# Kernel optimization log

Measured on AMD Instinct MI355X. Metric: run time of the kernel, lower is better.

The kernel has to match this reference:

```python
import jax, jax.numpy as jnp
import numpy as np

B, T, L, R, E, F = 8, 16, 128, 1024, 5, 512
# range(min_dist_exp, max_dist_exp+1) with 0 removed, per Diffusion.__init__
DIST_EXPONENTS = jnp.array([-3.0, -2.0, -1.0, 1.0, 2.0], dtype=jnp.float32)


def setup_inputs() -> dict:
    key = jax.random.key(0)
    ks = jax.random.split(key, 8)
    return {
        "lig_feat": jax.random.normal(ks[0], (B, L, E, F), jnp.float32) * 0.1,
        "rec_feat": jax.random.normal(ks[1], (B, R, E, F), jnp.float32) * 0.1,
        # coords on ~angstrom scale so negative-power distances stay bounded
        "lig_coord": jax.random.normal(ks[2], (B, L, 3), jnp.float32) * 5.0,
        "rec_coord": jax.random.normal(ks[3], (B, R, 3), jnp.float32) * 5.0,
        "pre_rot": jax.random.normal(ks[4], (B, T, 3, 3), jnp.float32),
        "trans": jax.random.normal(ks[5], (B, T, 3), jnp.float32),
        "lig_counts": jax.random.randint(ks[6], (B,), L // 2, L + 1, jnp.int32),
        "rec_counts": jax.random.randint(ks[7], (B,), R // 2, R + 1, jnp.int32),
    }


def reference(lig_feat, rec_feat, lig_coord, rec_coord, pre_rot, trans,
              lig_counts, rec_counts):
    # get_energy over a ragged batch (padded + masked), vectorized over
    # graphs (b) and timesteps (t). rot = QR(pre_rot) as in energy_grad.
    exps = DIST_EXPONENTS.astype(lig_feat.dtype)          # [E]
    rot = jnp.linalg.qr(pre_rot)[0]                       # [B,T,3,3]
    # einsum('nij,bj->nbi', rot, lig_coord) + trans, batched over graphs
    new_lig = jnp.einsum('btij,blj->btli', rot, lig_coord) + trans[:, :, None, :]  # [B,T,L,3]

    lig_mask = jnp.arange(lig_coord.shape[1]) < lig_counts[:, None]   # [B,L]
    rec_mask = jnp.arange(rec_coord.shape[1]) < rec_counts[:, None]   # [B,R]
    pair_mask = lig_mask[:, :, None] & rec_mask[:, None, :]           # [B,L,R]

    # atn_coefs = einsum('lef,ref->lre'); zero out padded pairs
    atn = jnp.einsum('blef,bref->blre', lig_feat, rec_feat) * pair_mask[..., None]  # [B,L,R,E]

    diff = new_lig[:, :, :, None, :] - rec_coord[:, None, None, :, :]  # [B,T,L,R,3]
    dists = jnp.sqrt(jnp.sum(diff * diff, axis=-1))                    # [B,T,L,R]
    # padded pairs -> 1.0 so negative exponents don't produce inf*0
    dists = jnp.where(pair_mask[:, None, :, :], dists, 1.0)
    dist_exp = dists[..., None] ** exps                                # [B,T,L,R,E]

    U = jnp.einsum('blre,btlre->bt', atn, dist_exp)                    # [B,T]
    return U
```

## Files before the change

kernel.cpp:

```cpp
#include <hip/hip_runtime.h>
#include <hip/hip_bf16.h>

#define B_ 8
#define T_ 16
#define L_ 128
#define R_ 1024
#define E_ 5
#define F_ 512

typedef short short8 __attribute__((ext_vector_type(8)));
typedef float floatx4 __attribute__((ext_vector_type(4)));
typedef unsigned short ushort4v __attribute__((ext_vector_type(4)));

__device__ __forceinline__ unsigned short f2bf(float f) {
  unsigned u = __float_as_uint(f);
  return (unsigned short)((u + 0x8000u) >> 16);
}

__device__ __forceinline__ short8 pack8(floatx4 lo, floatx4 hi) {
  short8 v;
  v[0] = (short)f2bf(lo[0]); v[1] = (short)f2bf(lo[1]);
  v[2] = (short)f2bf(lo[2]); v[3] = (short)f2bf(lo[3]);
  v[4] = (short)f2bf(hi[0]); v[5] = (short)f2bf(hi[1]);
  v[6] = (short)f2bf(hi[2]); v[7] = (short)f2bf(hi[3]);
  return v;
}

__device__ __forceinline__ void stage16(const float* g, float* lds) {
  __builtin_amdgcn_global_load_lds(
      (const __attribute__((address_space(1))) void*)g,
      (__attribute__((address_space(3))) void*)lds, 16, 0, 0);
}

#define WAITCNT_VM6 0xF76
#define WAITCNT_VM0 0xF70

__global__ void prep_kernel(const float* __restrict__ lig_coord,
                            const float* __restrict__ pre_rot,
                            const float* __restrict__ trans,
                            float* __restrict__ new_lig) {
  int bt = blockIdx.x;
  __shared__ float Qs[3][3];
  if (threadIdx.x == 0) {
    float a[3][3], q[3][3];
    #pragma unroll
    for (int i = 0; i < 3; ++i)
      #pragma unroll
      for (int j = 0; j < 3; ++j) {
        a[i][j] = pre_rot[(bt * 3 + i) * 3 + j];
        q[i][j] = (i == j) ? 1.f : 0.f;
      }
    for (int k = 0; k < 3; ++k) {
      float alpha = a[k][k];
      float xn2 = 0.f;
      for (int i = k + 1; i < 3; ++i) xn2 += a[i][k] * a[i][k];
      float nrm = sqrtf(alpha * alpha + xn2);
      if (xn2 > 0.f && nrm > 0.f) {
        float beta = (alpha >= 0.f) ? -nrm : nrm;
        float tau = (beta - alpha) / beta;
        float inv = 1.f / (alpha - beta);
        float v[3] = {0.f, 0.f, 0.f};
        v[k] = 1.f;
        for (int i = k + 1; i < 3; ++i) v[i] = a[i][k] * inv;
        for (int j = k; j < 3; ++j) {
          float w = 0.f;
          for (int i = k; i < 3; ++i) w += v[i] * a[i][j];
          w *= tau;
          for (int i = k; i < 3; ++i) a[i][j] -= w * v[i];
        }
        for (int i = 0; i < 3; ++i) {
          float w = 0.f;
          for (int j = k; j < 3; ++j) w += q[i][j] * v[j];
          w *= tau;
          for (int j = k; j < 3; ++j) q[i][j] -= w * v[j];
        }
      }
    }
    for (int i = 0; i < 3; ++i)
      for (int j = 0; j < 3; ++j) Qs[i][j] = q[i][j];
  }
  __syncthreads();
  int b = bt >> 4;
  int l = threadIdx.x;
  float cx = lig_coord[(b * L_ + l) * 3 + 0];
  float cy = lig_coord[(b * L_ + l) * 3 + 1];
  float cz = lig_coord[(b * L_ + l) * 3 + 2];
  float nx = Qs[0][0] * cx + Qs[0][1] * cy + Qs[0][2] * cz + trans[bt * 3 + 0];
  float ny = Qs[1][0] * cx + Qs[1][1] * cy + Qs[1][2] * cz + trans[bt * 3 + 1];
  float nz = Qs[2][0] * cx + Qs[2][1] * cy + Qs[2][2] * cz + trans[bt * 3 + 2];
  float* o = new_lig + ((size_t)bt * L_ + l) * 3;
  o[0] = nx; o[1] = ny; o[2] = nz;
}

__launch_bounds__(256)
__global__ void gemm_kernel(const float* __restrict__ lig_feat,
                            const float* __restrict__ rec_feat,
                            const int* __restrict__ rec_counts,
                            unsigned short* __restrict__ atn) {
  const int rt = blockIdx.x;
  const int e  = blockIdx.y;
  const int b  = blockIdx.z;
  const int r0 = rt * 64;
  if (r0 >= rec_counts[b]) return;

  __shared__ float As[2][128 * 32];
  __shared__ float Bs[2][64 * 32];

  const int tid  = threadIdx.x;
  const int wave = tid >> 6;
  const int lane = tid & 63;
  const int lrow = lane & 15;
  const int quad = lane >> 4;
  const int wm   = wave * 32;

  const int lr8 = lane >> 3;
  const int sw  = (lane & 7) ^ lr8;
  const float* ga[4];
  #pragma unroll
  for (int i = 0; i < 4; ++i) {
    int row = wave * 32 + i * 8 + lr8;
    ga[i] = lig_feat + ((size_t)(b * L_ + row) * E_ + e) * F_ + sw * 4;
  }
  const float* gb[2];
  #pragma unroll
  for (int i = 0; i < 2; ++i) {
    int row = wave * 16 + i * 8 + lr8;
    gb[i] = rec_feat + ((size_t)(b * R_ + r0 + row) * E_ + e) * F_ + sw * 4;
  }

  floatx4 acc[2][4];
  #pragma unroll
  for (int i = 0; i < 2; ++i)
    #pragma unroll
    for (int j = 0; j < 4; ++j)
      acc[i][j] = (floatx4){0.f, 0.f, 0.f, 0.f};

  const int c0 = (2 * quad) ^ (lane & 7);

  #pragma unroll
  for (int i = 0; i < 4; ++i) stage16(ga[i], &As[0][(wave * 32 + i * 8) * 32]);
  #pragma unroll
  for (int i = 0; i < 2; ++i) stage16(gb[i], &Bs[0][(wave * 16 + i * 8) * 32]);

  #pragma unroll 1
  for (int kc = 0; kc < 16; ++kc) {
    const int cur = kc & 1;
    if (kc > 0)
      __builtin_amdgcn_s_barrier();
    if (kc < 15) {
      const int col = (kc + 1) * 32;
      #pragma unroll
      for (int i = 0; i < 4; ++i)
        stage16(ga[i] + col, &As[cur ^ 1][(wave * 32 + i * 8) * 32]);
      #pragma unroll
      for (int i = 0; i < 2; ++i)
        stage16(gb[i] + col, &Bs[cur ^ 1][(wave * 16 + i * 8) * 32]);
      __builtin_amdgcn_s_waitcnt(WAITCNT_VM6);
    } else {
      __builtin_amdgcn_s_waitcnt(WAITCNT_VM0);
    }
    __builtin_amdgcn_s_barrier();
    __builtin_amdgcn_sched_barrier(0);

    short8 af[2], bfv[4];
    #pragma unroll
    for (int i = 0; i < 2; ++i) {
      const float* base = &As[cur][(wm + i * 16 + lrow) * 32];
      af[i] = pack8(*(const floatx4*)(base + c0 * 4),
                    *(const floatx4*)(base + (c0 ^ 1) * 4));
    }
    #pragma unroll
    for (int j = 0; j < 4; ++j) {
      const float* base = &Bs[cur][(j * 16 + lrow) * 32];
      bfv[j] = pack8(*(const floatx4*)(base + c0 * 4),
                     *(const floatx4*)(base + (c0 ^ 1) * 4));
    }
    #pragma unroll
    for (int i = 0; i < 2; ++i)
      #pragma unroll
      for (int j = 0; j < 4; ++j)
        acc[i][j] = __builtin_amdgcn_mfma_f32_16x16x32_bf16(af[i], bfv[j], acc[i][j], 0, 0, 0);
  }

  const size_t base = (size_t)(b * E_ + e) * L_ * R_;
  #pragma unroll
  for (int i = 0; i < 2; ++i)
    #pragma unroll
    for (int j = 0; j < 4; ++j)
      #pragma unroll
      for (int reg = 0; reg < 4; ++reg) {
        int m = wm + i * 16 + quad * 4 + reg;
        int n = j * 16 + lrow;
        atn[base + (size_t)m * R_ + r0 + n] = f2bf(acc[i][j][reg]);
      }
}

__launch_bounds__(256)
__global__ void reduce_kernel(const unsigned short* __restrict__ atn,
                              const float* __restrict__ new_lig,
                              const float* __restrict__ rec_coord,
                              const int* __restrict__ lig_counts,
                              const int* __restrict__ rec_counts,
                              float* __restrict__ partial) {
  const int b = blockIdx.x >> 7;
  const int l = blockIdx.x & 127;
  const int tid = threadIdx.x;
  if (l >= lig_counts[b]) {
    if (tid < T_) partial[(size_t)(b * T_ + tid) * L_ + l] = 0.f;
    return;
  }
  const int recN = rec_counts[b];
  const int wave = tid >> 6;

  __shared__ float nl[T_][3];
  __shared__ float sm[4][T_];
  if (tid < T_ * 3)
    nl[tid / 3][tid % 3] =
        new_lig[((size_t)(b * T_ + tid / 3) * L_ + l) * 3 + (tid % 3)];
  __syncthreads();

  float u[T_];
  #pragma unroll
  for (int t = 0; t < T_; ++t) u[t] = 0.f;

  if (wave * 256 < recN) {
    const int r = tid * 4;
    const size_t plane = (size_t)L_ * R_;
    const unsigned short* atnB = atn + (size_t)b * E_ * plane + (size_t)l * R_ + r;
    const float* rcB = rec_coord + ((size_t)b * R_ + r) * 3;

    ushort4v a4[5];
    #pragma unroll
    for (int e = 0; e < 5; ++e) a4[e] = *(const ushort4v*)(atnB + e * plane);
    floatx4 q0 = *(const floatx4*)(rcB + 0);
    floatx4 q1 = *(const floatx4*)(rcB + 4);
    floatx4 q2 = *(const floatx4*)(rcB + 8);
    float px[4] = {q0[0], q0[3], q1[2], q2[1]};
    float py[4] = {q0[1], q1[0], q1[3], q2[2]};
    float pz[4] = {q0[2], q1[1], q2[0], q2[3]};
    float am[5][4];
    #pragma unroll
    for (int e = 0; e < 5; ++e)
      #pragma unroll
      for (int s = 0; s < 4; ++s)
        am[e][s] = (r + s < recN)
                       ? __uint_as_float((unsigned)a4[e][s] << 16)
                       : 0.f;

    #pragma unroll
    for (int t = 0; t < T_; ++t) {
      float acc = 0.f;
      #pragma unroll
      for (int s = 0; s < 4; ++s) {
        float dx = nl[t][0] - px[s];
        float dy = nl[t][1] - py[s];
        float dz = nl[t][2] - pz[s];
        float d2 = fmaf(dx, dx, fmaf(dy, dy, dz * dz));
        d2 = fmaxf(d2, 1e-20f);
        float rs  = rsqrtf(d2);
        float rs2 = rs * rs;
        float rs3 = rs2 * rs;
        float d1  = d2 * rs;
        float c = am[0][s] * rs3;
        c = fmaf(am[1][s], rs2, c);
        c = fmaf(am[2][s], rs, c);
        c = fmaf(am[3][s], d1, c);
        c = fmaf(am[4][s], d2, c);
        acc += c;
      }
      u[t] += acc;
    }
  }

  #pragma unroll
  for (int t = 0; t < T_; ++t) {
    float v = u[t];
    #pragma unroll
    for (int m = 32; m > 0; m >>= 1) v += __shfl_xor(v, m, 64);
    if ((tid & 63) == 0) sm[wave][t] = v;
  }
  __syncthreads();
  if (tid < T_)
    partial[(size_t)(b * T_ + tid) * L_ + l] =
        sm[0][tid] + sm[1][tid] + sm[2][tid] + sm[3][tid];
}

__global__ void final_kernel(const float* __restrict__ partial,
                             float* __restrict__ out) {
  const int bt = blockIdx.x;
  const int l = threadIdx.x;
  float v = partial[(size_t)bt * L_ + l];
  #pragma unroll
  for (int m = 32; m > 0; m >>= 1) v += __shfl_xor(v, m, 64);
  __shared__ float s[2];
  if ((l & 63) == 0) s[l >> 6] = v;
  __syncthreads();
  if (l == 0) out[bt] = s[0] + s[1];
}

extern "C" void kernel_launch(void* const* d_in, const int* in_sizes, int n_in,
                              void* d_out, int out_size, void* d_ws, size_t ws_size,
                              hipStream_t stream) {
  const float* lig_feat   = (const float*)d_in[0];
  const float* rec_feat   = (const float*)d_in[1];
  const float* lig_coord  = (const float*)d_in[2];
  const float* rec_coord  = (const float*)d_in[3];
  const float* pre_rot    = (const float*)d_in[4];
  const float* trans      = (const float*)d_in[5];
  const int*   lig_counts = (const int*)d_in[6];
  const int*   rec_counts = (const int*)d_in[7];
  float* out = (float*)d_out;

  float* new_lig = (float*)d_ws;
  unsigned short* atn = (unsigned short*)(new_lig + (size_t)B_ * T_ * L_ * 3);
  float* partial = (float*)(atn + (size_t)B_ * E_ * L_ * R_);

  prep_kernel<<<dim3(B_ * T_), dim3(L_), 0, stream>>>(lig_coord, pre_rot, trans, new_lig);
  gemm_kernel<<<dim3(R_ / 64, E_, B_), dim3(256), 0, stream>>>(lig_feat, rec_feat,
                                                               rec_counts, atn);
  reduce_kernel<<<dim3(B_ * L_), dim3(256), 0, stream>>>(atn, new_lig, rec_coord,
                                                         lig_counts, rec_counts, partial);
  final_kernel<<<dim3(B_ * T_), dim3(128), 0, stream>>>(partial, out);
}
```

Before: 167.5 us.

## Fuse attention GEMM with distance-energy reduction and atomically accumulate output

Merges the bf16 MFMA GEMM and the distance-power reduction into one kernel. Each block computes all five exponent channels for a 128x32 ligand-receptor tile, keeps the results in registers, and evaluates the energy terms directly, so the bf16 atn intermediate is never written to or read from global memory. Per-block sums are added into the output with atomicAdd after prep zeroes it, which removes the partial and final kernels. The trade-off is fewer, larger blocks (256 instead of 640 GEMM blocks) that each run a longer sequential K loop, plus heavier register pressure from holding the accumulators of all five channels.

New measurement: 212.4 us. 1.27x slower.

```diff
diff --git a/kernel.cpp b/kernel.cpp
--- a/kernel.cpp
+++ b/kernel.cpp
@@ -1,5 +1,4 @@
 #include <hip/hip_runtime.h>
-#include <hip/hip_bf16.h>
 
 #define B_ 8
 #define T_ 16
@@ -10,7 +9,6 @@
 
 typedef short short8 __attribute__((ext_vector_type(8)));
 typedef float floatx4 __attribute__((ext_vector_type(4)));
-typedef unsigned short ushort4v __attribute__((ext_vector_type(4)));
 
 __device__ __forceinline__ unsigned short f2bf(float f) {
   unsigned u = __float_as_uint(f);
@@ -32,16 +30,19 @@
       (__attribute__((address_space(3))) void*)lds, 16, 0, 0);
 }
 
-#define WAITCNT_VM6 0xF76
+#define WAITCNT_VM3 0xF73
+#define WAITCNT_VM2 0xF72
 #define WAITCNT_VM0 0xF70
 
 __global__ void prep_kernel(const float* __restrict__ lig_coord,
                             const float* __restrict__ pre_rot,
                             const float* __restrict__ trans,
-                            float* __restrict__ new_lig) {
+                            float* __restrict__ new_lig,
+                            float* __restrict__ out) {
   int bt = blockIdx.x;
   __shared__ float Qs[3][3];
   if (threadIdx.x == 0) {
+    out[bt] = 0.f;
     float a[3][3], q[3][3];
     #pragma unroll
     for (int i = 0; i < 3; ++i)
@@ -92,184 +93,165 @@
   o[0] = nx; o[1] = ny; o[2] = nz;
 }
 
-__launch_bounds__(256)
-__global__ void gemm_kernel(const float* __restrict__ lig_feat,
-                            const float* __restrict__ rec_feat,
-                            const int* __restrict__ rec_counts,
-                            unsigned short* __restrict__ atn) {
+__launch_bounds__(512)
+__global__ void fused_kernel(const float* __restrict__ lig_feat,
+                             const float* __restrict__ rec_feat,
+                             const float* __restrict__ rec_coord,
+                             const int* __restrict__ lig_counts,
+                             const int* __restrict__ rec_counts,
+                             const float* __restrict__ new_lig,
+                             float* __restrict__ out) {
   const int rt = blockIdx.x;
-  const int e  = blockIdx.y;
-  const int b  = blockIdx.z;
-  const int r0 = rt * 64;
-  if (r0 >= rec_counts[b]) return;
-
-  __shared__ float As[2][128 * 32];
-  __shared__ float Bs[2][64 * 32];
+  const int b  = blockIdx.y;
+  const int r0 = rt * 32;
+  const int recN = rec_counts[b];
+  if (r0 >= recN) return;
+
+  __shared__ __align__(16) float smem[2 * 128 * 32 + 2 * 32 * 32];
+  __shared__ float smr[8][T_];
+  float* const As0 = smem;
+  float* const Bs0 = smem + 2 * 128 * 32;
 
   const int tid  = threadIdx.x;
   const int wave = tid >> 6;
   const int lane = tid & 63;
   const int lrow = lane & 15;
   const int quad = lane >> 4;
-  const int wm   = wave * 32;
+  const int wm   = wave * 16;
 
   const int lr8 = lane >> 3;
   const int sw  = (lane & 7) ^ lr8;
-  const float* ga[4];
-  #pragma unroll
-  for (int i = 0; i < 4; ++i) {
-    int row = wave * 32 + i * 8 + lr8;
-    ga[i] = lig_feat + ((size_t)(b * L_ + row) * E_ + e) * F_ + sw * 4;
-  }
-  const float* gb[2];
+  const bool bwave = (wave < 4);
+
+  const float* ga[2];
   #pragma unroll
   for (int i = 0; i < 2; ++i) {
     int row = wave * 16 + i * 8 + lr8;
-    gb[i] = rec_feat + ((size_t)(b * R_ + r0 + row) * E_ + e) * F_ + sw * 4;
-  }
-
-  floatx4 acc[2][4];
-  #pragma unroll
-  for (int i = 0; i < 2; ++i)
-    #pragma unroll
-    for (int j = 0; j < 4; ++j)
-      acc[i][j] = (floatx4){0.f, 0.f, 0.f, 0.f};
+    ga[i] = lig_feat + ((size_t)(b * L_ + row) * E_) * F_ + sw * 4;
+  }
+  const float* gb = rec_feat +
+      ((size_t)(b * R_ + r0 + wave * 8 + lr8) * E_) * F_ + sw * 4;
+
+  const int dstA0 = (wave * 16 + 0) * 32;
+  const int dstA1 = (wave * 16 + 8) * 32;
+  const int dstB  = (wave * 8) * 32;
+
+  floatx4 acc[E_][2];
+  #pragma unroll
+  for (int e = 0; e < E_; ++e)
+    #pragma unroll
+    for (int j = 0; j < 2; ++j)
+      acc[e][j] = (floatx4){0.f, 0.f, 0.f, 0.f};
+
+  stage16(ga[0], As0 + dstA0);
+  stage16(ga[1], As0 + dstA1);
+  if (bwave) stage16(gb, Bs0 + dstB);
 
   const int c0 = (2 * quad) ^ (lane & 7);
 
   #pragma unroll
-  for (int i = 0; i < 4; ++i) stage16(ga[i], &As[0][(wave * 32 + i * 8) * 32]);
-  #pragma unroll
-  for (int i = 0; i < 2; ++i) stage16(gb[i], &Bs[0][(wave * 16 + i * 8) * 32]);
-
-  #pragma unroll 1
-  for (int kc = 0; kc < 16; ++kc) {
-    const int cur = kc & 1;
-    if (kc > 0)
+  for (int e = 0; e < E_; ++e) {
+    #pragma unroll 1
+    for (int kc = 0; kc < 16; ++kc) {
+      const int g = e * 16 + kc;
+      const int cur = g & 1;
+      if (g > 0)
+        __builtin_amdgcn_s_barrier();
+      if (g < 79) {
+        const int col = (g + 1) * 32;
+        stage16(ga[0] + col, As0 + (cur ^ 1) * (128 * 32) + dstA0);
+        stage16(ga[1] + col, As0 + (cur ^ 1) * (128 * 32) + dstA1);
+        if (bwave) {
+          stage16(gb + col, Bs0 + (cur ^ 1) * (32 * 32) + dstB);
+          __builtin_amdgcn_s_waitcnt(WAITCNT_VM3);
+        } else {
+          __builtin_amdgcn_s_waitcnt(WAITCNT_VM2);
+        }
+      } else {
+        __builtin_amdgcn_s_waitcnt(WAITCNT_VM0);
+      }
       __builtin_amdgcn_s_barrier();
-    if (kc < 15) {
-      const int col = (kc + 1) * 32;
-      #pragma unroll
-      for (int i = 0; i < 4; ++i)
-        stage16(ga[i] + col, &As[cur ^ 1][(wave * 32 + i * 8) * 32]);
-      #pragma unroll
-      for (int i = 0; i < 2; ++i)
-        stage16(gb[i] + col, &Bs[cur ^ 1][(wave * 16 + i * 8) * 32]);
-      __builtin_amdgcn_s_waitcnt(WAITCNT_VM6);
-    } else {
-      __builtin_amdgcn_s_waitcnt(WAITCNT_VM0);
-    }
-    __builtin_amdgcn_s_barrier();
-    __builtin_amdgcn_sched_barrier(0);
-
-    short8 af[2], bfv[4];
-    #pragma unroll
-    for (int i = 0; i < 2; ++i) {
-      const float* base = &As[cur][(wm + i * 16 + lrow) * 32];
-      af[i] = pack8(*(const floatx4*)(base + c0 * 4),
-                    *(const floatx4*)(base + (c0 ^ 1) * 4));
-    }
-    #pragma unroll
-    for (int j = 0; j < 4; ++j) {
-      const float* base = &Bs[cur][(j * 16 + lrow) * 32];
-      bfv[j] = pack8(*(const floatx4*)(base + c0 * 4),
-                     *(const floatx4*)(base + (c0 ^ 1) * 4));
-    }
-    #pragma unroll
-    for (int i = 0; i < 2; ++i)
-      #pragma unroll
-      for (int j = 0; j < 4; ++j)
-        acc[i][j] = __builtin_amdgcn_mfma_f32_16x16x32_bf16(af[i], bfv[j], acc[i][j], 0, 0, 0);
-  }
-
-  const size_t base = (size_t)(b * E_ + e) * L_ * R_;
-  #pragma unroll
-  for (int i = 0; i < 2; ++i)
-    #pragma unroll
-    for (int j = 0; j < 4; ++j)
+      __builtin_amdgcn_sched_barrier(0);
+
+      const float* abase = As0 + cur * (128 * 32) + (wm + lrow) * 32;
+      short8 af = pack8(*(const floatx4*)(abase + c0 * 4),
+                        *(const floatx4*)(abase + (c0 ^ 1) * 4));
+      const float* bbase0 = Bs0 + cur * (32 * 32) + (lrow) * 32;
+      const float* bbase1 = Bs0 + cur * (32 * 32) + (16 + lrow) * 32;
+      short8 bf0 = pack8(*(const floatx4*)(bbase0 + c0 * 4),
+                         *(const floatx4*)(bbase0 + (c0 ^ 1) * 4));
+      short8 bf1 = pack8(*(const floatx4*)(bbase1 + c0 * 4),
+                         *(const floatx4*)(bbase1 + (c0 ^ 1) * 4));
+      acc[e][0] = __builtin_amdgcn_mfma_f32_16x16x32_bf16(af, bf0, acc[e][0], 0, 0, 0);
+      acc[e][1] = __builtin_amdgcn_mfma_f32_16x16x32_bf16(af, bf1, acc[e][1], 0, 0, 0);
+    }
+  }
+
+  __syncthreads();
+
+
+  float* const nlp = smem;
+  {
+    const floatx4* src = (const floatx4*)(new_lig + (size_t)b * T_ * L_ * 3);
+    floatx4* dst = (floatx4*)nlp;
+    #pragma unroll
+    for (int i = 0; i < 3; ++i) dst[tid + i * 512] = src[tid + i * 512];
+  }
+  __syncthreads();
+
+  const int ligN = lig_counts[b];
+  #pragma unroll
+  for (int j = 0; j < 2; ++j) {
+    const bool nv = (r0 + j * 16 + lrow) < recN;
+    #pragma unroll
+    for (int reg = 0; reg < 4; ++reg) {
+      const bool mv = (wm + quad * 4 + reg) < ligN;
+      if (!(nv && mv)) {
+        #pragma unroll
+        for (int e = 0; e < E_; ++e) acc[e][j][reg] = 0.f;
+      }
+    }
+  }
+
+  float rcx[2], rcy[2], rcz[2];
+  #pragma unroll
+  for (int j = 0; j < 2; ++j) {
+    const float* rp = rec_coord + (size_t)(b * R_ + r0 + j * 16 + lrow) * 3;
+    rcx[j] = rp[0]; rcy[j] = rp[1]; rcz[j] = rp[2];
+  }
+
+  float u[T_];
+  #pragma unroll
+  for (int t = 0; t < T_; ++t) u[t] = 0.f;
+
+  #pragma unroll
+  for (int t = 0; t < T_; ++t) {
+    float nx[4], ny[4], nz[4];
+    #pragma unroll
+    for (int reg = 0; reg < 4; ++reg) {
+      const float* np = nlp + ((t * L_) + wm + quad * 4 + reg) * 3;
+      nx[reg] = np[0]; ny[reg] = np[1]; nz[reg] = np[2];
+    }
+    #pragma unroll
+    for (int j = 0; j < 2; ++j)
       #pragma unroll
       for (int reg = 0; reg < 4; ++reg) {
-        int m = wm + i * 16 + quad * 4 + reg;
-        int n = j * 16 + lrow;
-        atn[base + (size_t)m * R_ + r0 + n] = f2bf(acc[i][j][reg]);
-      }
-}
-
-__launch_bounds__(256)
-__global__ void reduce_kernel(const unsigned short* __restrict__ atn,
-                              const float* __restrict__ new_lig,
-                              const float* __restrict__ rec_coord,
-                              const int* __restrict__ lig_counts,
-                              const int* __restrict__ rec_counts,
-                              float* __restrict__ partial) {
-  const int b = blockIdx.x >> 7;
-  const int l = blockIdx.x & 127;
-  const int tid = threadIdx.x;
-  if (l >= lig_counts[b]) {
-    if (tid < T_) partial[(size_t)(b * T_ + tid) * L_ + l] = 0.f;
-    return;
-  }
-  const int recN = rec_counts[b];
-  const int wave = tid >> 6;
-
-  __shared__ float nl[T_][3];
-  __shared__ float sm[4][T_];
-  if (tid < T_ * 3)
-    nl[tid / 3][tid % 3] =
-        new_lig[((size_t)(b * T_ + tid / 3) * L_ + l) * 3 + (tid % 3)];
-  __syncthreads();
-
-  float u[T_];
-  #pragma unroll
-  for (int t = 0; t < T_; ++t) u[t] = 0.f;
-
-  if (wave * 256 < recN) {
-    const int r = tid * 4;
-    const size_t plane = (size_t)L_ * R_;
-    const unsigned short* atnB = atn + (size_t)b * E_ * plane + (size_t)l * R_ + r;
-    const float* rcB = rec_coord + ((size_t)b * R_ + r) * 3;
-
-    ushort4v a4[5];
-    #pragma unroll
-    for (int e = 0; e < 5; ++e) a4[e] = *(const ushort4v*)(atnB + e * plane);
-    floatx4 q0 = *(const floatx4*)(rcB + 0);
-    floatx4 q1 = *(const floatx4*)(rcB + 4);
-    floatx4 q2 = *(const floatx4*)(rcB + 8);
-    float px[4] = {q0[0], q0[3], q1[2], q2[1]};
-    float py[4] = {q0[1], q1[0], q1[3], q2[2]};
-    float pz[4] = {q0[2], q1[1], q2[0], q2[3]};
-    float am[5][4];
-    #pragma unroll
-    for (int e = 0; e < 5; ++e)
-      #pragma unroll
-      for (int s = 0; s < 4; ++s)
-        am[e][s] = (r + s < recN)
-                       ? __uint_as_float((unsigned)a4[e][s] << 16)
-                       : 0.f;
-
-    #pragma unroll
-    for (int t = 0; t < T_; ++t) {
-      float acc = 0.f;
-      #pragma unroll
-      for (int s = 0; s < 4; ++s) {
-        float dx = nl[t][0] - px[s];
-        float dy = nl[t][1] - py[s];
-        float dz = nl[t][2] - pz[s];
+        float dx = nx[reg] - rcx[j];
+        float dy = ny[reg] - rcy[j];
+        float dz = nz[reg] - rcz[j];
         float d2 = fmaf(dx, dx, fmaf(dy, dy, dz * dz));
         d2 = fmaxf(d2, 1e-20f);
         float rs  = rsqrtf(d2);
         float rs2 = rs * rs;
         float rs3 = rs2 * rs;
         float d1  = d2 * rs;
-        float c = am[0][s] * rs3;
-        c = fmaf(am[1][s], rs2, c);
-        c = fmaf(am[2][s], rs, c);
-        c = fmaf(am[3][s], d1, c);
-        c = fmaf(am[4][s], d2, c);
-        acc += c;
-      }
-      u[t] += acc;
-    }
+        float c = acc[0][j][reg] * rs3;
+        c = fmaf(acc[1][j][reg], rs2, c);
+        c = fmaf(acc[2][j][reg], rs,  c);
+        c = fmaf(acc[3][j][reg], d1,  c);
+        c = fmaf(acc[4][j][reg], d2,  c);
+        u[t] += c;
+      }
   }
 
   #pragma unroll
@@ -277,25 +259,15 @@
     float v = u[t];
     #pragma unroll
     for (int m = 32; m > 0; m >>= 1) v += __shfl_xor(v, m, 64);
-    if ((tid & 63) == 0) sm[wave][t] = v;
-  }
-  __syncthreads();
-  if (tid < T_)
-    partial[(size_t)(b * T_ + tid) * L_ + l] =
-        sm[0][tid] + sm[1][tid] + sm[2][tid] + sm[3][tid];
-}
-
-__global__ void final_kernel(const float* __restrict__ partial,
-                             float* __restrict__ out) {
-  const int bt = blockIdx.x;
-  const int l = threadIdx.x;
-  float v = partial[(size_t)bt * L_ + l];
-  #pragma unroll
-  for (int m = 32; m > 0; m >>= 1) v += __shfl_xor(v, m, 64);
-  __shared__ float s[2];
-  if ((l & 63) == 0) s[l >> 6] = v;
-  __syncthreads();
-  if (l == 0) out[bt] = s[0] + s[1];
+    if (lane == 0) smr[wave][t] = v;
+  }
+  __syncthreads();
+  if (tid < T_) {
+    float s = 0.f;
+    #pragma unroll
+    for (int w = 0; w < 8; ++w) s += smr[w][tid];
+    atomicAdd(&out[b * T_ + tid], s);
+  }
 }
 
 extern "C" void kernel_launch(void* const* d_in, const int* in_sizes, int n_in,
@@ -312,13 +284,9 @@
   float* out = (float*)d_out;
 
   float* new_lig = (float*)d_ws;
-  unsigned short* atn = (unsigned short*)(new_lig + (size_t)B_ * T_ * L_ * 3);
-  float* partial = (float*)(atn + (size_t)B_ * E_ * L_ * R_);
-
-  prep_kernel<<<dim3(B_ * T_), dim3(L_), 0, stream>>>(lig_coord, pre_rot, trans, new_lig);
-  gemm_kernel<<<dim3(R_ / 64, E_, B_), dim3(256), 0, stream>>>(lig_feat, rec_feat,
-                                                               rec_counts, atn);
-  reduce_kernel<<<dim3(B_ * L_), dim3(256), 0, stream>>>(atn, new_lig, rec_coord,
-                                                         lig_counts, rec_counts, partial);
-  final_kernel<<<dim3(B_ * T_), dim3(128), 0, stream>>>(partial, out);
-}
+
+  prep_kernel<<<dim3(B_ * T_), dim3(L_), 0, stream>>>(lig_coord, pre_rot, trans,
+                                                      new_lig, out);
+  fused_kernel<<<dim3(R_ / 32, B_), dim3(512), 0, stream>>>(
+      lig_feat, rec_feat, rec_coord, lig_counts, rec_counts, new_lig, out);
+}
```

## Fuse distance-power reduction into GEMM epilogue with atomic output accumulation

Applied to the files above, without the earlier changes.

Removes the bf16 attention intermediate and the separate reduce and final kernels. Each GEMM block now computes distance powers for its own exponent directly on the MFMA accumulators and accumulates per-timestep sums into the output with atomics. The output is zeroed in the prep kernel. This avoids writing and re-reading the 10 MB atn buffer and cuts two launches, but it adds redundant distance computation per exponent block, LDS staging of new_lig, syncthreads per timestep group, and float atomics with nondeterministic summation order.

Result: slower. 180.5 us (+7.7%).

```diff
diff --git a/kernel.cpp b/kernel.cpp
--- a/kernel.cpp
+++ b/kernel.cpp
@@ -1,5 +1,4 @@
 #include <hip/hip_runtime.h>
-#include <hip/hip_bf16.h>
 
 #define B_ 8
 #define T_ 16
@@ -10,7 +9,6 @@
 
 typedef short short8 __attribute__((ext_vector_type(8)));
 typedef float floatx4 __attribute__((ext_vector_type(4)));
-typedef unsigned short ushort4v __attribute__((ext_vector_type(4)));
 
 __device__ __forceinline__ unsigned short f2bf(float f) {
   unsigned u = __float_as_uint(f);
@@ -38,10 +36,12 @@
 __global__ void prep_kernel(const float* __restrict__ lig_coord,
                             const float* __restrict__ pre_rot,
                             const float* __restrict__ trans,
-                            float* __restrict__ new_lig) {
+                            float* __restrict__ new_lig,
+                            float* __restrict__ out) {
   int bt = blockIdx.x;
   __shared__ float Qs[3][3];
   if (threadIdx.x == 0) {
+    out[bt] = 0.f;
     float a[3][3], q[3][3];
     #pragma unroll
     for (int i = 0; i < 3; ++i)
@@ -92,19 +92,75 @@
   o[0] = nx; o[1] = ny; o[2] = nz;
 }
 
+template <int EIDX>
+__device__ __forceinline__ void phaseB(const floatx4 (&acc)[2][4],
+                                       const float* nlp,
+                                       const float (&rcx)[4],
+                                       const float (&rcy)[4],
+                                       const float (&rcz)[4],
+                                       int wm, int quad, int lane, int wave,
+                                       float (*smr)[T_]) {
+  #pragma unroll 1
+  for (int tg = 0; tg < 4; ++tg) {
+    #pragma unroll
+    for (int it = 0; it < 4; ++it) {
+      const int t = tg * 4 + it;
+      float uacc = 0.f;
+      #pragma unroll
+      for (int i = 0; i < 2; ++i)
+        #pragma unroll
+        for (int reg = 0; reg < 4; ++reg) {
+          const int m = wm + i * 16 + quad * 4 + reg;
+          const float* np = nlp + (t * L_ + m) * 3;
+          const float nx = np[0], ny = np[1], nz = np[2];
+          #pragma unroll
+          for (int j = 0; j < 4; ++j) {
+            float dx = nx - rcx[j];
+            float dy = ny - rcy[j];
+            float dz = nz - rcz[j];
+            float d2 = fmaf(dx, dx, fmaf(dy, dy, dz * dz));
+            d2 = fmaxf(d2, 1e-20f);
+            float p;
+            if constexpr (EIDX == 0) {
+              float rs = rsqrtf(d2); p = rs * rs * rs;
+            } else if constexpr (EIDX == 1) {
+              float rs = rsqrtf(d2); p = rs * rs;
+            } else if constexpr (EIDX == 2) {
+              p = rsqrtf(d2);
+            } else if constexpr (EIDX == 3) {
+              float rs = rsqrtf(d2); p = d2 * rs;
+            } else {
+              p = d2;
+            }
+            uacc = fmaf(acc[i][j][reg], p, uacc);
+          }
+        }
+      #pragma unroll
+      for (int m_ = 32; m_ > 0; m_ >>= 1) uacc += __shfl_xor(uacc, m_, 64);
+      if (lane == 0) smr[wave][t] = uacc;
+    }
+    __syncthreads();
+  }
+}
+
 __launch_bounds__(256)
-__global__ void gemm_kernel(const float* __restrict__ lig_feat,
-                            const float* __restrict__ rec_feat,
-                            const int* __restrict__ rec_counts,
-                            unsigned short* __restrict__ atn) {
+__global__ void fused_kernel(const float* __restrict__ lig_feat,
+                             const float* __restrict__ rec_feat,
+                             const float* __restrict__ rec_coord,
+                             const int* __restrict__ lig_counts,
+                             const int* __restrict__ rec_counts,
+                             const float* __restrict__ new_lig,
+                             float* __restrict__ out) {
   const int rt = blockIdx.x;
   const int e  = blockIdx.y;
   const int b  = blockIdx.z;
   const int r0 = rt * 64;
-  if (r0 >= rec_counts[b]) return;
-
-  __shared__ float As[2][128 * 32];
-  __shared__ float Bs[2][64 * 32];
+  const int recN = rec_counts[b];
+  if (r0 >= recN) return;
+
+  __shared__ __align__(16) float As[2][128 * 32];
+  __shared__ __align__(16) float Bs[2][64 * 32];
+  __shared__ float smr[4][T_];
 
   const int tid  = threadIdx.x;
   const int wave = tid >> 6;
@@ -182,120 +238,49 @@
         acc[i][j] = __builtin_amdgcn_mfma_f32_16x16x32_bf16(af[i], bfv[j], acc[i][j], 0, 0, 0);
   }
 
-  const size_t base = (size_t)(b * E_ + e) * L_ * R_;
-  #pragma unroll
-  for (int i = 0; i < 2; ++i)
-    #pragma unroll
-    for (int j = 0; j < 4; ++j)
+  __syncthreads();
+
+
+  float* const nlp = &As[0][0];
+  {
+    const floatx4* src = (const floatx4*)(new_lig + (size_t)b * T_ * L_ * 3);
+    floatx4* dst = (floatx4*)nlp;
+    #pragma unroll
+    for (int i = 0; i < 6; ++i) dst[tid + i * 256] = src[tid + i * 256];
+  }
+  __syncthreads();
+
+  const int ligN = lig_counts[b];
+  #pragma unroll
+  for (int j = 0; j < 4; ++j) {
+    const bool nv = (r0 + j * 16 + lrow) < recN;
+    #pragma unroll
+    for (int i = 0; i < 2; ++i)
       #pragma unroll
       for (int reg = 0; reg < 4; ++reg) {
-        int m = wm + i * 16 + quad * 4 + reg;
-        int n = j * 16 + lrow;
-        atn[base + (size_t)m * R_ + r0 + n] = f2bf(acc[i][j][reg]);
+        const bool mv = (wm + i * 16 + quad * 4 + reg) < ligN;
+        if (!(nv && mv)) acc[i][j][reg] = 0.f;
       }
-}
-
-__launch_bounds__(256)
-__global__ void reduce_kernel(const unsigned short* __restrict__ atn,
-                              const float* __restrict__ new_lig,
-                              const float* __restrict__ rec_coord,
-                              const int* __restrict__ lig_counts,
-                              const int* __restrict__ rec_counts,
-                              float* __restrict__ partial) {
-  const int b = blockIdx.x >> 7;
-  const int l = blockIdx.x & 127;
-  const int tid = threadIdx.x;
-  if (l >= lig_counts[b]) {
-    if (tid < T_) partial[(size_t)(b * T_ + tid) * L_ + l] = 0.f;
-    return;
-  }
-  const int recN = rec_counts[b];
-  const int wave = tid >> 6;
-
-  __shared__ float nl[T_][3];
-  __shared__ float sm[4][T_];
-  if (tid < T_ * 3)
-    nl[tid / 3][tid % 3] =
-        new_lig[((size_t)(b * T_ + tid / 3) * L_ + l) * 3 + (tid % 3)];
+  }
+
+  float rcx[4], rcy[4], rcz[4];
+  #pragma unroll
+  for (int j = 0; j < 4; ++j) {
+    const float* rp = rec_coord + (size_t)(b * R_ + r0 + j * 16 + lrow) * 3;
+    rcx[j] = rp[0]; rcy[j] = rp[1]; rcz[j] = rp[2];
+  }
+
+  if (e == 0)      phaseB<0>(acc, nlp, rcx, rcy, rcz, wm, quad, lane, wave, smr);
+  else if (e == 1) phaseB<1>(acc, nlp, rcx, rcy, rcz, wm, quad, lane, wave, smr);
+  else if (e == 2) phaseB<2>(acc, nlp, rcx, rcy, rcz, wm, quad, lane, wave, smr);
+  else if (e == 3) phaseB<3>(acc, nlp, rcx, rcy, rcz, wm, quad, lane, wave, smr);
+  else             phaseB<4>(acc, nlp, rcx, rcy, rcz, wm, quad, lane, wave, smr);
+
   __syncthreads();
-
-  float u[T_];
-  #pragma unroll
-  for (int t = 0; t < T_; ++t) u[t] = 0.f;
-
-  if (wave * 256 < recN) {
-    const int r = tid * 4;
-    const size_t plane = (size_t)L_ * R_;
-    const unsigned short* atnB = atn + (size_t)b * E_ * plane + (size_t)l * R_ + r;
-    const float* rcB = rec_coord + ((size_t)b * R_ + r) * 3;
-
-    ushort4v a4[5];
-    #pragma unroll
-    for (int e = 0; e < 5; ++e) a4[e] = *(const ushort4v*)(atnB + e * plane);
-    floatx4 q0 = *(const floatx4*)(rcB + 0);
-    floatx4 q1 = *(const floatx4*)(rcB + 4);
-    floatx4 q2 = *(const floatx4*)(rcB + 8);
-    float px[4] = {q0[0], q0[3], q1[2], q2[1]};
-    float py[4] = {q0[1], q1[0], q1[3], q2[2]};
-    float pz[4] = {q0[2], q1[1], q2[0], q2[3]};
-    float am[5][4];
-    #pragma unroll
-    for (int e = 0; e < 5; ++e)
-      #pragma unroll
-      for (int s = 0; s < 4; ++s)
-        am[e][s] = (r + s < recN)
-                       ? __uint_as_float((unsigned)a4[e][s] << 16)
-                       : 0.f;
-
-    #pragma unroll
-    for (int t = 0; t < T_; ++t) {
-      float acc = 0.f;
-      #pragma unroll
-      for (int s = 0; s < 4; ++s) {
-        float dx = nl[t][0] - px[s];
-        float dy = nl[t][1] - py[s];
-        float dz = nl[t][2] - pz[s];
-        float d2 = fmaf(dx, dx, fmaf(dy, dy, dz * dz));
-        d2 = fmaxf(d2, 1e-20f);
-        float rs  = rsqrtf(d2);
-        float rs2 = rs * rs;
-        float rs3 = rs2 * rs;
-        float d1  = d2 * rs;
-        float c = am[0][s] * rs3;
-        c = fmaf(am[1][s], rs2, c);
-        c = fmaf(am[2][s], rs, c);
-        c = fmaf(am[3][s], d1, c);
-        c = fmaf(am[4][s], d2, c);
-        acc += c;
-      }
-      u[t] += acc;
-    }
-  }
-
-  #pragma unroll
-  for (int t = 0; t < T_; ++t) {
-    float v = u[t];
-    #pragma unroll
-    for (int m = 32; m > 0; m >>= 1) v += __shfl_xor(v, m, 64);
-    if ((tid & 63) == 0) sm[wave][t] = v;
-  }
-  __syncthreads();
-  if (tid < T_)
-    partial[(size_t)(b * T_ + tid) * L_ + l] =
-        sm[0][tid] + sm[1][tid] + sm[2][tid] + sm[3][tid];
-}
-
-__global__ void final_kernel(const float* __restrict__ partial,
-                             float* __restrict__ out) {
-  const int bt = blockIdx.x;
-  const int l = threadIdx.x;
-  float v = partial[(size_t)bt * L_ + l];
-  #pragma unroll
-  for (int m = 32; m > 0; m >>= 1) v += __shfl_xor(v, m, 64);
-  __shared__ float s[2];
-  if ((l & 63) == 0) s[l >> 6] = v;
-  __syncthreads();
-  if (l == 0) out[bt] = s[0] + s[1];
+  if (tid < T_) {
+    float s = smr[0][tid] + smr[1][tid] + smr[2][tid] + smr[3][tid];
+    atomicAdd(&out[b * T_ + tid], s);
+  }
 }
 
 extern "C" void kernel_launch(void* const* d_in, const int* in_sizes, int n_in,
@@ -312,13 +297,9 @@
   float* out = (float*)d_out;
 
   float* new_lig = (float*)d_ws;
-  unsigned short* atn = (unsigned short*)(new_lig + (size_t)B_ * T_ * L_ * 3);
-  float* partial = (float*)(atn + (size_t)B_ * E_ * L_ * R_);
-
-  prep_kernel<<<dim3(B_ * T_), dim3(L_), 0, stream>>>(lig_coord, pre_rot, trans, new_lig);
-  gemm_kernel<<<dim3(R_ / 64, E_, B_), dim3(256), 0, stream>>>(lig_feat, rec_feat,
-                                                               rec_counts, atn);
-  reduce_kernel<<<dim3(B_ * L_), dim3(256), 0, stream>>>(atn, new_lig, rec_coord,
-                                                         lig_counts, rec_counts, partial);
-  final_kernel<<<dim3(B_ * T_), dim3(128), 0, stream>>>(partial, out);
-}
+
+  prep_kernel<<<dim3(B_ * T_), dim3(L_), 0, stream>>>(lig_coord, pre_rot, trans,
+                                                      new_lig, out);
+  fused_kernel<<<dim3(R_ / 64, E_, B_), dim3(256), 0, stream>>>(
+      lig_feat, rec_feat, rec_coord, lig_counts, rec_counts, new_lig, out);
+}
```
